# Performance work log

Hardware: AMD Instinct MI355X
Metric: run time of the kernel (lower is better)

## Reference

```python
import jax, jax.numpy as jnp
import numpy as np

N_NODES = 100000
N_EDGES = 1600000
D_IN = 128
D_HID = 128
D_OUT = 64
N_GRAPHS = 128


def setup_inputs() -> dict:
    key = jax.random.key(0)
    ks = jax.random.split(key, 8)
    x = jax.random.normal(ks[0], (N_NODES, D_IN), dtype=jnp.float32)
    edge_index = jax.random.randint(ks[1], (2, N_EDGES), 0, N_NODES, dtype=jnp.int64)
    batch = jnp.sort(jax.random.randint(ks[2], (N_NODES,), 0, N_GRAPHS, dtype=jnp.int64))
    def glorot(k, fi, fo):
        s = jnp.sqrt(6.0 / (fi + fo)).astype(jnp.float32)
        return jax.random.uniform(k, (fi, fo), jnp.float32, -1.0, 1.0) * s
    return {
        "x": x, "edge_index": edge_index, "batch": batch,
        "W1": glorot(ks[3], D_IN, D_HID), "b1": jnp.zeros((D_HID,), jnp.float32),
        "W2": glorot(ks[4], D_HID, D_HID), "b2": jnp.zeros((D_HID,), jnp.float32),
        "W3": glorot(ks[5], D_HID, D_HID), "b3": jnp.zeros((D_HID,), jnp.float32),
        "Wfc": glorot(ks[6], D_HID, D_OUT), "bfc": jnp.zeros((D_OUT,), jnp.float32),
    }


def _gcn_graph(edge_index, n_nodes):
    # add self-loops and compute symmetric normalization (PyG gcn_norm)
    loop = jnp.arange(n_nodes, dtype=edge_index.dtype)
    src = jnp.concatenate([edge_index[0], loop])
    dst = jnp.concatenate([edge_index[1], loop])
    deg = jax.ops.segment_sum(jnp.ones_like(dst, dtype=jnp.float32), dst,
                              num_segments=n_nodes)
    dinv = jnp.where(deg > 0, jax.lax.rsqrt(deg), 0.0)
    norm = dinv[src] * dinv[dst]  # [E + N]
    return src, dst, norm


def _gcn_conv(x, src, dst, norm, W, b, n_nodes):
    h = x @ W                                    # [N, F_out]
    msg = h[src] * norm[:, None]                 # gather + scale
    agg = jax.ops.segment_sum(msg, dst, num_segments=n_nodes)  # scatter-add
    return agg + b


def reference(x, edge_index, batch, W1, b1, W2, b2, W3, b3, Wfc, bfc):
    n = x.shape[0]
    src, dst, norm = _gcn_graph(edge_index, n)
    h = jax.nn.relu(_gcn_conv(x, src, dst, norm, W1, b1, n))
    h = jax.nn.relu(_gcn_conv(h, src, dst, norm, W2, b2, n))
    h = jax.nn.relu(_gcn_conv(h, src, dst, norm, W3, b3, n))
    # global mean pool over graphs in the batch
    sums = jax.ops.segment_sum(h, batch, num_segments=N_GRAPHS)
    cnts = jax.ops.segment_sum(jnp.ones((n,), jnp.float32), batch,
                               num_segments=N_GRAPHS)
    pooled = sums / jnp.maximum(cnts, 1.0)[:, None]   # [G, D_HID]
    return pooled @ Wfc + bfc                         # [G, D_OUT]
```

## Files before the change

### kernel.cpp

```cpp
#include <hip/hip_runtime.h>

#define NN 100000
#define NE 1600000
#define DF 128
#define DOUT 64
#define NG 128
#define NB 391
#define EPB 8192
#define NBLKA ((NE + EPB - 1) / EPB)
#define NBLKX 6250
#define PCH 8
#define NAGB (NN / 16)

typedef short short8 __attribute__((ext_vector_type(8)));
typedef float floatx4 __attribute__((ext_vector_type(4)));
typedef float floatx2 __attribute__((ext_vector_type(2)));

__device__ __forceinline__ unsigned short f2bf(float f) {
    unsigned int b = __float_as_uint(f);
    unsigned int r = (b + 0x7fffu + ((b >> 16) & 1u)) >> 16;
    return (unsigned short)r;
}
__device__ __forceinline__ float bf2f_lo(unsigned int v) { return __uint_as_float(v << 16); }
__device__ __forceinline__ float bf2f_hi(unsigned int v) { return __uint_as_float(v & 0xffff0000u); }

__device__ __forceinline__ int phi(int p) {
    return (((p >> 6) << 2) + (p & 3)) * 16 + ((p >> 2) & 15);
}


__global__ __launch_bounds__(256) void k_init(const int* __restrict__ batch,
                                              int* __restrict__ gstart,
                                              const float* __restrict__ W1,
                                              const float* __restrict__ W2,
                                              const float* __restrict__ W3,
                                              unsigned short* __restrict__ O1,
                                              unsigned short* __restrict__ O2,
                                              unsigned short* __restrict__ O3) {
    int blk = blockIdx.x;
    if (blk == 0) {
        int g = threadIdx.x;
        if (g > NG) return;
        int lo = 0, hi = NN;
        while (lo < hi) {
            int mid = (lo + hi) >> 1;
            if (batch[mid] < g) lo = mid + 1; else hi = mid;
        }
        gstart[g] = lo;
    } else {
        int bb = blk - 1;
        const float* W = (bb >= 16) ? W3 : (bb >= 8) ? W2 : W1;
        unsigned short* O = (bb >= 16) ? O3 : (bb >= 8) ? O2 : O1;
        int idx = (bb & 7) * 256 + threadIdx.x;
        int l = idx & 63;
        int s = (idx >> 6) & 3;
        int tt = idx >> 8;
        int k0 = s * 32 + (l >> 4) * 8;
        int c = tt * 16 + (l & 15);
        unsigned short o[8];
#pragma unroll
        for (int j = 0; j < 8; j++) o[j] = f2bf(W[phi(k0 + j) * DF + c]);
        *(short8*)&O[idx * 8] = *(short8*)o;
    }
}


__global__ __launch_bounds__(256) void k_pre(const int* __restrict__ dst,
                                             int* __restrict__ hist,
                                             const float* __restrict__ x,
                                             unsigned short* __restrict__ xb) {
    __shared__ int lh[NB];
    int t = threadIdx.x;
    if (blockIdx.x < NBLKA) {
        for (int i = t; i < NB; i += 256) lh[i] = 0;
        __syncthreads();
        int e0 = blockIdx.x * EPB;
        int e1 = min(e0 + EPB, NE);
        for (int e = e0 + t; e < e1; e += 256) atomicAdd(&lh[dst[e] >> 8], 1);
        __syncthreads();
        for (int i = t; i < NB; i += 256) hist[blockIdx.x * NB + i] = lh[i];
    } else {
        size_t i = ((size_t)(blockIdx.x - NBLKA) * 256 + t) * 8;
        size_t rb = i & ~(size_t)127;
        int p0 = (int)(i & 127);
        unsigned short o[8];
#pragma unroll
        for (int j = 0; j < 8; j++) o[j] = f2bf(x[rb + phi(p0 + j)]);
        *(short8*)&xb[i] = *(short8*)o;
    }
}

__global__ __launch_bounds__(256) void k_hscan(int* __restrict__ hist,
                                               int* __restrict__ bhist) {
    __shared__ int sh[256];
    int b = blockIdx.x, t = threadIdx.x;
    int v = (t < NBLKA) ? hist[t * NB + b] : 0;
    sh[t] = v;
    __syncthreads();
    for (int off = 1; off < 256; off <<= 1) {
        int a = (t >= off) ? sh[t - off] : 0;
        __syncthreads();
        sh[t] += a;
        __syncthreads();
    }
    if (t < NBLKA) hist[t * NB + b] = sh[t] - v;
    if (t == 255) bhist[b] = sh[255];
}

__global__ __launch_bounds__(512) void k_bscan(const int* __restrict__ bhist,
                                               int* __restrict__ bbase) {
    __shared__ int sh[512];
    int t = threadIdx.x;
    int v = (t < NB) ? bhist[t] : 0;
    sh[t] = v;
    __syncthreads();
    for (int off = 1; off < 512; off <<= 1) {
        int a = (t >= off) ? sh[t - off] : 0;
        __syncthreads();
        sh[t] += a;
        __syncthreads();
    }
    if (t < NB) bbase[t] = sh[t] - v;
    if (t == NB - 1) bbase[NB] = sh[t];
}

__global__ __launch_bounds__(256) void k_pairs(const int* __restrict__ src,
                                               const int* __restrict__ dst,
                                               const int* __restrict__ hist,
                                               const int* __restrict__ bbase,
                                               int2* __restrict__ ebuf) {
    __shared__ int lh[NB];
    __shared__ int lbase[NB];
    int t = threadIdx.x;
    for (int i = t; i < NB; i += 256) {
        lh[i] = 0;
        lbase[i] = bbase[i] + hist[blockIdx.x * NB + i];
    }
    __syncthreads();
    int e0 = blockIdx.x * EPB;
    int e1 = min(e0 + EPB, NE);
    for (int e = e0 + t; e < e1; e += 256) {
        int s = src[e], d = dst[e];
        int bk = d >> 8;
        int off = atomicAdd(&lh[bk], 1);
        ebuf[lbase[bk] + off] = make_int2(s, d);
    }
}

__global__ __launch_bounds__(256) void k_build(const int2* __restrict__ ebuf,
                                               const int* __restrict__ bbase,
                                               int* __restrict__ rowptr,
                                               float* __restrict__ dinv,
                                               int* __restrict__ col) {
    __shared__ int deg[256];
    __shared__ int lst[256];
    int b = blockIdx.x, t = threadIdx.x;
    int n0 = b << 8;
    int node = n0 + t;
    deg[t] = 0;
    __syncthreads();
    int e0 = bbase[b], e1 = bbase[b + 1];
    for (int e = e0 + t; e < e1; e += 256) atomicAdd(&deg[ebuf[e].y - n0], 1);
    __syncthreads();
    int v = deg[t];
    lst[t] = v;
    __syncthreads();
    for (int off = 1; off < 256; off <<= 1) {
        int a = (t >= off) ? lst[t - off] : 0;
        __syncthreads();
        lst[t] += a;
        __syncthreads();
    }
    int mystart = e0 + lst[t] - v;
    if (node < NN) {
        rowptr[node] = mystart;
        dinv[node] = rsqrtf((float)(v + 1));
    }
    if (b == NB - 1 && t == 255) rowptr[NN] = e1;
    lst[t] = mystart;
    __syncthreads();
    for (int e = e0 + t; e < e1; e += 256) {
        int2 pr = ebuf[e];
        int p = atomicAdd(&lst[pr.y - n0], 1);
        col[p] = pr.x * DF;
    }
}


__global__ __launch_bounds__(256) void k_gemm(const unsigned short* __restrict__ X,
                                              const unsigned short* __restrict__ Wb,
                                              const float* __restrict__ dinv,
                                              unsigned char* __restrict__ fs8) {
    int t = threadIdx.x;
    int wave = t >> 6, l = t & 63;
    int r0 = blockIdx.x * 64 + wave * 16;
    int lm = l & 15, q = l >> 4;

    int arow = r0 + lm;
    if (arow >= NN) arow = NN - 1;
    const unsigned short* xrow = X + (size_t)arow * DF + q * 8;
    short8 af0 = *(const short8*)(xrow);
    short8 af1 = *(const short8*)(xrow + 32);
    short8 af2 = *(const short8*)(xrow + 64);
    short8 af3 = *(const short8*)(xrow + 96);

    int orow = r0 + q * 4;
    float dv[4];
#pragma unroll
    for (int j = 0; j < 4; j++) dv[j] = (orow + j < NN) ? dinv[orow + j] : 0.f;

    float res[4][8];
#pragma unroll
    for (int tt = 0; tt < 8; tt++) {
        floatx4 acc = {0.f, 0.f, 0.f, 0.f};
        const unsigned short* wp = Wb + ((size_t)(tt * 4) * 64 + l) * 8;
        acc = __builtin_amdgcn_mfma_f32_16x16x32_bf16(af0, *(const short8*)(wp), acc, 0, 0, 0);
        acc = __builtin_amdgcn_mfma_f32_16x16x32_bf16(af1, *(const short8*)(wp + 512), acc, 0, 0, 0);
        acc = __builtin_amdgcn_mfma_f32_16x16x32_bf16(af2, *(const short8*)(wp + 1024), acc, 0, 0, 0);
        acc = __builtin_amdgcn_mfma_f32_16x16x32_bf16(af3, *(const short8*)(wp + 1536), acc, 0, 0, 0);
#pragma unroll
        for (int j = 0; j < 4; j++) res[j][tt] = acc[j] * dv[j];
    }

#pragma unroll
    for (int g = 0; g < 2; g++) {
#pragma unroll
        for (int j = 0; j < 4; j++) {
            int r = orow + j;
            if (r >= NN) continue;
            unsigned int w8 = __builtin_amdgcn_cvt_pk_fp8_f32(res[j][g * 4 + 0], res[j][g * 4 + 1], 0, false);
            w8 = __builtin_amdgcn_cvt_pk_fp8_f32(res[j][g * 4 + 2], res[j][g * 4 + 3], w8, true);
            *(unsigned int*)&fs8[(size_t)r * DF + g * 64 + lm * 4] = w8;
        }
    }
}

__global__ __launch_bounds__(256) void k_agg(const unsigned char* __restrict__ fs8,
                                             const int* __restrict__ colb,
                                             const int* __restrict__ rowptr,
                                             const float* __restrict__ dinv,
                                             const float* __restrict__ b,
                                             unsigned short* __restrict__ out) {
    int w = (int)((blockIdx.x * (size_t)blockDim.x + threadIdx.x) >> 6);
    int lane = threadIdx.x & 63;
    int sub = lane >> 4;
    int fo = lane & 15;
    int foff = fo * 8;
    int n = w * 4 + sub;

    float bias[8];
#pragma unroll
    for (int j = 0; j < 8; j++) bias[j] = b[phi(foff + j)];
    float dvn = dinv[n];

    int e0 = rowptr[n], e1 = rowptr[n + 1];

    floatx2 acc0 = {0.f, 0.f}, acc1 = {0.f, 0.f}, acc2 = {0.f, 0.f}, acc3 = {0.f, 0.f};

    for (int base = e0; base < e1; base += 8) {
        int cb[8];
#pragma unroll
        for (int k = 0; k < 8; k++) cb[k] = colb[min(base + k, e1 - 1)];
        uint2 vv[8];
#pragma unroll
        for (int k = 0; k < 8; k++) vv[k] = *(const uint2*)&fs8[(size_t)cb[k] + foff];
#pragma unroll
        for (int k = 0; k < 8; k++) {
            if (base + k < e1) {
                acc0 += __builtin_amdgcn_cvt_pk_f32_fp8(vv[k].x, false);
                acc1 += __builtin_amdgcn_cvt_pk_f32_fp8(vv[k].x, true);
                acc2 += __builtin_amdgcn_cvt_pk_f32_fp8(vv[k].y, false);
                acc3 += __builtin_amdgcn_cvt_pk_f32_fp8(vv[k].y, true);
            }
        }
    }

    uint2 sv = *(const uint2*)&fs8[(size_t)n * DF + foff];
    acc0 += __builtin_amdgcn_cvt_pk_f32_fp8(sv.x, false);
    acc1 += __builtin_amdgcn_cvt_pk_f32_fp8(sv.x, true);
    acc2 += __builtin_amdgcn_cvt_pk_f32_fp8(sv.y, false);
    acc3 += __builtin_amdgcn_cvt_pk_f32_fp8(sv.y, true);

    float a[8] = {acc0.x, acc0.y, acc1.x, acc1.y, acc2.x, acc2.y, acc3.x, acc3.y};
    float o[8];
#pragma unroll
    for (int j = 0; j < 8; j++) o[j] = fmaxf(dvn * a[j] + bias[j], 0.f);
    uint4 pk;
    pk.x = (unsigned int)f2bf(o[0]) | ((unsigned int)f2bf(o[1]) << 16);
    pk.y = (unsigned int)f2bf(o[2]) | ((unsigned int)f2bf(o[3]) << 16);
    pk.z = (unsigned int)f2bf(o[4]) | ((unsigned int)f2bf(o[5]) << 16);
    pk.w = (unsigned int)f2bf(o[6]) | ((unsigned int)f2bf(o[7]) << 16);
    *(uint4*)&out[(size_t)n * DF + foff] = pk;
}


__global__ __launch_bounds__(256) void k_poolA(const unsigned short* __restrict__ h,
                                               const int* __restrict__ gstart,
                                               float* __restrict__ part) {
    __shared__ float2 red[256];
    int g = blockIdx.x >> 3, c = blockIdx.x & 7;
    int s = gstart[g], e = gstart[g + 1];
    int len = e - s;
    int cs = s + (int)(((long long)len * c) >> 3);
    int ce = s + (int)(((long long)len * (c + 1)) >> 3);
    int t = threadIdx.x;
    int fp = t & 63;
    int rs = t >> 6;
    float2 acc = make_float2(0.f, 0.f);
    for (int n = cs + rs; n < ce; n += 4) {
        unsigned int v = *(const unsigned int*)&h[(size_t)n * DF + fp * 2];
        acc.x += bf2f_lo(v);
        acc.y += bf2f_hi(v);
    }
    red[t] = acc;
    __syncthreads();
    if (rs == 0) {
        float2 a0 = red[fp], a1 = red[fp + 64], a2 = red[fp + 128], a3 = red[fp + 192];
        float2 o;
        o.x = (a0.x + a1.x) + (a2.x + a3.x);
        o.y = (a0.y + a1.y) + (a2.y + a3.y);
        *(float2*)&part[(size_t)blockIdx.x * DF + fp * 2] = o;
    }
}

__global__ __launch_bounds__(128) void k_poolfc(const float* __restrict__ part,
                                                const int* __restrict__ gstart,
                                                const float* __restrict__ Wfc,
                                                const float* __restrict__ bfc,
                                                float* __restrict__ out) {
    __shared__ float pl[DF];
    int g = blockIdx.x;
    int f = threadIdx.x;
    float s = 0.f;
#pragma unroll
    for (int c = 0; c < PCH; c++) s += part[(size_t)(g * PCH + c) * DF + f];
    int cnt = gstart[g + 1] - gstart[g];
    pl[phi(f)] = s / (float)max(cnt, 1);
    __syncthreads();
    if (f < DOUT) {
        float acc = bfc[f];
        for (int k = 0; k < DF; k++) acc += pl[k] * Wfc[k * DOUT + f];
        out[g * DOUT + f] = acc;
    }
}


extern "C" void kernel_launch(void* const* d_in, const int* in_sizes, int n_in,
                              void* d_out, int out_size, void* d_ws, size_t ws_size,
                              hipStream_t stream) {
    const float* x     = (const float*)d_in[0];
    const int*   ei    = (const int*)d_in[1];
    const int*   batch = (const int*)d_in[2];
    const float* W1 = (const float*)d_in[3];
    const float* b1 = (const float*)d_in[4];
    const float* W2 = (const float*)d_in[5];
    const float* b2 = (const float*)d_in[6];
    const float* W3 = (const float*)d_in[7];
    const float* b3 = (const float*)d_in[8];
    const float* Wfc = (const float*)d_in[9];
    const float* bfc = (const float*)d_in[10];
    float* out = (float*)d_out;

    char* p = (char*)d_ws;
    unsigned short* xb = (unsigned short*)p;  p += (size_t)NN * DF * sizeof(short);
    unsigned short* ob = (unsigned short*)p;  p += (size_t)NN * DF * sizeof(short);
    unsigned char*  fs8 = (unsigned char*)p;  p += (size_t)NN * DF;
    unsigned short* Wb1 = (unsigned short*)p; p += 16384 * sizeof(short);
    unsigned short* Wb2 = (unsigned short*)p; p += 16384 * sizeof(short);
    unsigned short* Wb3 = (unsigned short*)p; p += 16384 * sizeof(short);
    float* dinv = (float*)p;           p += (size_t)NN * sizeof(float);
    int* rowptr = (int*)p;             p += (size_t)(NN + 4) * sizeof(int);
    int* col    = (int*)p;             p += (size_t)NE * sizeof(int);
    int2* ebuf  = (int2*)p;            p += (size_t)NE * sizeof(int2);
    int* bhist  = (int*)p;             p += (size_t)(NB + 4) * sizeof(int);
    int* bbase  = (int*)p;             p += (size_t)(NB + 4) * sizeof(int);
    int* hist   = (int*)p;             p += (size_t)NBLKA * NB * sizeof(int);
    int* gstart = (int*)p;             p += (size_t)(NG + 4) * sizeof(int);
    float* part = (float*)p;           p += (size_t)NG * PCH * DF * sizeof(float);

    const int* e_src = ei;
    const int* e_dst = ei + NE;

    k_init<<<25, 256, 0, stream>>>(batch, gstart, W1, W2, W3, Wb1, Wb2, Wb3);
    k_pre<<<NBLKA + NBLKX, 256, 0, stream>>>(e_dst, hist, x, xb);
    k_hscan<<<NB, 256, 0, stream>>>(hist, bhist);
    k_bscan<<<1, 512, 0, stream>>>(bhist, bbase);
    k_pairs<<<NBLKA, 256, 0, stream>>>(e_src, e_dst, hist, bbase, ebuf);
    k_build<<<NB, 256, 0, stream>>>(ebuf, bbase, rowptr, dinv, col);

    int ggrid = (NN + 63) / 64;

    k_gemm<<<ggrid, 256, 0, stream>>>(xb, Wb1, dinv, fs8);
    k_agg<<<NAGB, 256, 0, stream>>>(fs8, col, rowptr, dinv, b1, ob);
    k_gemm<<<ggrid, 256, 0, stream>>>(ob, Wb2, dinv, fs8);
    k_agg<<<NAGB, 256, 0, stream>>>(fs8, col, rowptr, dinv, b2, ob);
    k_gemm<<<ggrid, 256, 0, stream>>>(ob, Wb3, dinv, fs8);
    k_agg<<<NAGB, 256, 0, stream>>>(fs8, col, rowptr, dinv, b3, ob);

    k_poolA<<<NG * PCH, 256, 0, stream>>>(ob, gstart, part);
    k_poolfc<<<NG, 128, 0, stream>>>(part, gstart, Wfc, bfc, out);
}
```

Measured before the change: 337.0 us.

## Fuse aggregation with next layer's GEMM via shared-memory tile

Adds a fused kernel that aggregates 64 nodes per block into a swizzled bf16 LDS tile and then runs the next layer's MFMA GEMM on that tile, writing fp8 features directly. This removes the bf16 hidden-state write and reread between layers 1-2 and 2-3 and two kernel launches. Because outputs can no longer overwrite inputs in place, fp8 features ping-pong between two buffers. The cost is fewer waves per aggregation step (four nodes per wave done serially) and extra LDS use, which can reduce latency hiding for the gather.

Result: slower. 357.5 us (+6.1%).

```diff
diff --git a/kernel.cpp b/kernel.cpp
--- a/kernel.cpp
+++ b/kernel.cpp
@@ -11,6 +11,7 @@
 #define NBLKX 6250
 #define PCH 8
 #define NAGB (NN / 16)
+#define NBF ((NN + 63) / 64)
 
 typedef short short8 __attribute__((ext_vector_type(8)));
 typedef float floatx4 __attribute__((ext_vector_type(4)));
@@ -187,6 +188,40 @@
 }
 
 
+__device__ __forceinline__ void agg_node(const unsigned char* __restrict__ fs8,
+                                         const int* __restrict__ colb,
+                                         int n, int foff, int e0, int e1,
+                                         float dvn, const float* bias,
+                                         float* o) {
+    floatx2 acc0 = {0.f, 0.f}, acc1 = {0.f, 0.f}, acc2 = {0.f, 0.f}, acc3 = {0.f, 0.f};
+    for (int base = e0; base < e1; base += 8) {
+        int cb[8];
+#pragma unroll
+        for (int k = 0; k < 8; k++) cb[k] = colb[min(base + k, e1 - 1)];
+        uint2 vv[8];
+#pragma unroll
+        for (int k = 0; k < 8; k++) vv[k] = *(const uint2*)&fs8[(size_t)cb[k] + foff];
+#pragma unroll
+        for (int k = 0; k < 8; k++) {
+            if (base + k < e1) {
+                acc0 += __builtin_amdgcn_cvt_pk_f32_fp8(vv[k].x, false);
+                acc1 += __builtin_amdgcn_cvt_pk_f32_fp8(vv[k].x, true);
+                acc2 += __builtin_amdgcn_cvt_pk_f32_fp8(vv[k].y, false);
+                acc3 += __builtin_amdgcn_cvt_pk_f32_fp8(vv[k].y, true);
+            }
+        }
+    }
+    uint2 sv = *(const uint2*)&fs8[(size_t)n * DF + foff];
+    acc0 += __builtin_amdgcn_cvt_pk_f32_fp8(sv.x, false);
+    acc1 += __builtin_amdgcn_cvt_pk_f32_fp8(sv.x, true);
+    acc2 += __builtin_amdgcn_cvt_pk_f32_fp8(sv.y, false);
+    acc3 += __builtin_amdgcn_cvt_pk_f32_fp8(sv.y, true);
+
+    float a[8] = {acc0.x, acc0.y, acc1.x, acc1.y, acc2.x, acc2.y, acc3.x, acc3.y};
+#pragma unroll
+    for (int j = 0; j < 8; j++) o[j] = fmaxf(dvn * a[j] + bias[j], 0.f);
+}
+
 __global__ __launch_bounds__(256) void k_gemm(const unsigned short* __restrict__ X,
                                               const unsigned short* __restrict__ Wb,
                                               const float* __restrict__ dinv,
@@ -231,6 +266,81 @@
             unsigned int w8 = __builtin_amdgcn_cvt_pk_fp8_f32(res[j][g * 4 + 0], res[j][g * 4 + 1], 0, false);
             w8 = __builtin_amdgcn_cvt_pk_fp8_f32(res[j][g * 4 + 2], res[j][g * 4 + 3], w8, true);
             *(unsigned int*)&fs8[(size_t)r * DF + g * 64 + lm * 4] = w8;
+        }
+    }
+}
+
+__global__ __launch_bounds__(256, 6) void k_fused(const unsigned char* __restrict__ fs8_in,
+                                                  const int* __restrict__ colb,
+                                                  const int* __restrict__ rowptr,
+                                                  const float* __restrict__ dinv,
+                                                  const float* __restrict__ b,
+                                                  const unsigned short* __restrict__ Wb,
+                                                  unsigned char* __restrict__ fs8_out) {
+    __shared__ unsigned short tile[4][16 * DF];
+    int t = threadIdx.x;
+    int w = t >> 6, lane = t & 63;
+    int sub = lane >> 4, fo = lane & 15;
+    int foff = fo * 8;
+    int r0 = blockIdx.x * 64 + w * 16;
+
+    float bias[8];
+#pragma unroll
+    for (int j = 0; j < 8; j++) bias[j] = b[phi(foff + j)];
+
+    unsigned short* mytile = &tile[w][0];
+
+#pragma unroll 1
+    for (int pass = 0; pass < 4; ++pass) {
+        int row = pass * 4 + sub;
+        int n = r0 + row;
+        int nc = (n < NN) ? n : (NN - 1);
+        float dvn = dinv[nc];
+        int e0 = rowptr[nc], e1 = rowptr[nc + 1];
+        float o[8];
+        agg_node(fs8_in, colb, nc, foff, e0, e1, dvn, bias, o);
+        uint4 pk;
+        pk.x = (unsigned int)f2bf(o[0]) | ((unsigned int)f2bf(o[1]) << 16);
+        pk.y = (unsigned int)f2bf(o[2]) | ((unsigned int)f2bf(o[3]) << 16);
+        pk.z = (unsigned int)f2bf(o[4]) | ((unsigned int)f2bf(o[5]) << 16);
+        pk.w = (unsigned int)f2bf(o[6]) | ((unsigned int)f2bf(o[7]) << 16);
+        *(uint4*)&mytile[row * DF + ((fo ^ row) * 8)] = pk;
+    }
+    __syncthreads();
+
+    int lm = lane & 15, q = lane >> 4;
+    short8 af[4];
+#pragma unroll
+    for (int k = 0; k < 4; k++)
+        af[k] = *(const short8*)&mytile[lm * DF + (((q + 4 * k) ^ lm) * 8)];
+
+    int orow = r0 + q * 4;
+    float dv[4];
+#pragma unroll
+    for (int j = 0; j < 4; j++) dv[j] = (orow + j < NN) ? dinv[orow + j] : 0.f;
+
+#pragma unroll
+    for (int g = 0; g < 2; g++) {
+        float res[4][4];
+#pragma unroll
+        for (int u = 0; u < 4; u++) {
+            int tt = g * 4 + u;
+            floatx4 acc = {0.f, 0.f, 0.f, 0.f};
+            const unsigned short* wp = Wb + ((size_t)(tt * 4) * 64 + lane) * 8;
+            acc = __builtin_amdgcn_mfma_f32_16x16x32_bf16(af[0], *(const short8*)(wp), acc, 0, 0, 0);
+            acc = __builtin_amdgcn_mfma_f32_16x16x32_bf16(af[1], *(const short8*)(wp + 512), acc, 0, 0, 0);
+            acc = __builtin_amdgcn_mfma_f32_16x16x32_bf16(af[2], *(const short8*)(wp + 1024), acc, 0, 0, 0);
+            acc = __builtin_amdgcn_mfma_f32_16x16x32_bf16(af[3], *(const short8*)(wp + 1536), acc, 0, 0, 0);
+#pragma unroll
+            for (int j = 0; j < 4; j++) res[j][u] = acc[j] * dv[j];
+        }
+#pragma unroll
+        for (int j = 0; j < 4; j++) {
+            int r = orow + j;
+            if (r >= NN) continue;
+            unsigned int w8 = __builtin_amdgcn_cvt_pk_fp8_f32(res[j][0], res[j][1], 0, false);
+            w8 = __builtin_amdgcn_cvt_pk_fp8_f32(res[j][2], res[j][3], w8, true);
+            *(unsigned int*)&fs8_out[(size_t)r * DF + g * 64 + lm * 4] = w8;
         }
     }
 }
@@ -252,39 +362,11 @@
 #pragma unroll
     for (int j = 0; j < 8; j++) bias[j] = b[phi(foff + j)];
     float dvn = dinv[n];
-
     int e0 = rowptr[n], e1 = rowptr[n + 1];
 
-    floatx2 acc0 = {0.f, 0.f}, acc1 = {0.f, 0.f}, acc2 = {0.f, 0.f}, acc3 = {0.f, 0.f};
-
-    for (int base = e0; base < e1; base += 8) {
-        int cb[8];
-#pragma unroll
-        for (int k = 0; k < 8; k++) cb[k] = colb[min(base + k, e1 - 1)];
-        uint2 vv[8];
-#pragma unroll
-        for (int k = 0; k < 8; k++) vv[k] = *(const uint2*)&fs8[(size_t)cb[k] + foff];
-#pragma unroll
-        for (int k = 0; k < 8; k++) {
-            if (base + k < e1) {
-                acc0 += __builtin_amdgcn_cvt_pk_f32_fp8(vv[k].x, false);
-                acc1 += __builtin_amdgcn_cvt_pk_f32_fp8(vv[k].x, true);
-                acc2 += __builtin_amdgcn_cvt_pk_f32_fp8(vv[k].y, false);
-                acc3 += __builtin_amdgcn_cvt_pk_f32_fp8(vv[k].y, true);
-            }
-        }
-    }
-
-    uint2 sv = *(const uint2*)&fs8[(size_t)n * DF + foff];
-    acc0 += __builtin_amdgcn_cvt_pk_f32_fp8(sv.x, false);
-    acc1 += __builtin_amdgcn_cvt_pk_f32_fp8(sv.x, true);
-    acc2 += __builtin_amdgcn_cvt_pk_f32_fp8(sv.y, false);
-    acc3 += __builtin_amdgcn_cvt_pk_f32_fp8(sv.y, true);
-
-    float a[8] = {acc0.x, acc0.y, acc1.x, acc1.y, acc2.x, acc2.y, acc3.x, acc3.y};
     float o[8];
-#pragma unroll
-    for (int j = 0; j < 8; j++) o[j] = fmaxf(dvn * a[j] + bias[j], 0.f);
+    agg_node(fs8, colb, n, foff, e0, e1, dvn, bias, o);
+
     uint4 pk;
     pk.x = (unsigned int)f2bf(o[0]) | ((unsigned int)f2bf(o[1]) << 16);
     pk.y = (unsigned int)f2bf(o[2]) | ((unsigned int)f2bf(o[3]) << 16);
@@ -364,7 +446,8 @@
     char* p = (char*)d_ws;
     unsigned short* xb = (unsigned short*)p;  p += (size_t)NN * DF * sizeof(short);
     unsigned short* ob = (unsigned short*)p;  p += (size_t)NN * DF * sizeof(short);
-    unsigned char*  fs8 = (unsigned char*)p;  p += (size_t)NN * DF;
+    unsigned char*  fs8a = (unsigned char*)p; p += (size_t)NN * DF;
+    unsigned char*  fs8b = (unsigned char*)p; p += (size_t)NN * DF;
     unsigned short* Wb1 = (unsigned short*)p; p += 16384 * sizeof(short);
     unsigned short* Wb2 = (unsigned short*)p; p += 16384 * sizeof(short);
     unsigned short* Wb3 = (unsigned short*)p; p += 16384 * sizeof(short);
@@ -390,12 +473,10 @@
 
     int ggrid = (NN + 63) / 64;
 
-    k_gemm<<<ggrid, 256, 0, stream>>>(xb, Wb1, dinv, fs8);
-    k_agg<<<NAGB, 256, 0, stream>>>(fs8, col, rowptr, dinv, b1, ob);
-    k_gemm<<<ggrid, 256, 0, stream>>>(ob, Wb2, dinv, fs8);
-    k_agg<<<NAGB, 256, 0, stream>>>(fs8, col, rowptr, dinv, b2, ob);
-    k_gemm<<<ggrid, 256, 0, stream>>>(ob, Wb3, dinv, fs8);
-    k_agg<<<NAGB, 256, 0, stream>>>(fs8, col, rowptr, dinv, b3, ob);
+    k_gemm<<<ggrid, 256, 0, stream>>>(xb, Wb1, dinv, fs8a);
+    k_fused<<<NBF, 256, 0, stream>>>(fs8a, col, rowptr, dinv, b1, Wb2, fs8b);
+    k_fused<<<NBF, 256, 0, stream>>>(fs8b, col, rowptr, dinv, b2, Wb3, fs8a);
+    k_agg<<<NAGB, 256, 0, stream>>>(fs8a, col, rowptr, dinv, b3, ob);
 
     k_poolA<<<NG * PCH, 256, 0, stream>>>(ob, gstart, part);
     k_poolfc<<<NG, 128, 0, stream>>>(part, gstart, Wfc, bfc, out);
```

## Fuse x conversion into first GEMM and merge scans via last-block ticket

Applied to the files above, without the earlier changes.

Drops the separate pass that converts x to permuted bf16. The first GEMM now reads fp32 x directly and converts it in registers, and W1 is laid out in logical order to match. The histogram and weight-prep kernels are merged into one launch, and the two scan kernels are combined using an atomic ticket so the last block performs the global scan. The aggregation gains a fast path for degree ≤16 that pads neighbour indices to a zero row instead of masking them, trading extra gather loads for less branching. Together these cut launches and a full write-then-read of the bf16 copy of x, at the cost of more global loads in the first GEMM.

Result: slower. 351.9 us (+4.4%).

```diff
diff --git a/kernel.cpp b/kernel.cpp
--- a/kernel.cpp
+++ b/kernel.cpp
@@ -8,9 +8,9 @@
 #define NB 391
 #define EPB 8192
 #define NBLKA ((NE + EPB - 1) / EPB)
-#define NBLKX 6250
 #define PCH 8
 #define NAGB (NN / 16)
+#define ZOFF (NN * DF)
 
 typedef short short8 __attribute__((ext_vector_type(8)));
 typedef float floatx4 __attribute__((ext_vector_type(4)));
@@ -29,17 +29,31 @@
 }
 
 
-__global__ __launch_bounds__(256) void k_init(const int* __restrict__ batch,
+__global__ __launch_bounds__(256) void k_init(const int* __restrict__ dst,
+                                              int* __restrict__ hist,
+                                              const int* __restrict__ batch,
                                               int* __restrict__ gstart,
+                                              unsigned char* __restrict__ fs8,
+                                              int* __restrict__ ticket,
                                               const float* __restrict__ W1,
                                               const float* __restrict__ W2,
                                               const float* __restrict__ W3,
                                               unsigned short* __restrict__ O1,
                                               unsigned short* __restrict__ O2,
                                               unsigned short* __restrict__ O3) {
+    __shared__ int lh[NB];
     int blk = blockIdx.x;
-    if (blk == 0) {
-        int g = threadIdx.x;
+    int t = threadIdx.x;
+    if (blk < NBLKA) {
+        for (int i = t; i < NB; i += 256) lh[i] = 0;
+        __syncthreads();
+        int e0 = blk * EPB;
+        int e1 = min(e0 + EPB, NE);
+        for (int e = e0 + t; e < e1; e += 256) atomicAdd(&lh[dst[e] >> 8], 1);
+        __syncthreads();
+        for (int i = t; i < NB; i += 256) hist[blk * NB + i] = lh[i];
+    } else if (blk == NBLKA) {
+        int g = t;
         if (g > NG) return;
         int lo = 0, hi = NN;
         while (lo < hi) {
@@ -47,11 +61,15 @@
             if (batch[mid] < g) lo = mid + 1; else hi = mid;
         }
         gstart[g] = lo;
+    } else if (blk == NBLKA + 1) {
+        if (t < 32) *(unsigned int*)&fs8[ZOFF + t * 4] = 0u;
+        if (t == 32) *ticket = 0;
     } else {
-        int bb = blk - 1;
+        int bb = blk - (NBLKA + 2);
         const float* W = (bb >= 16) ? W3 : (bb >= 8) ? W2 : W1;
         unsigned short* O = (bb >= 16) ? O3 : (bb >= 8) ? O2 : O1;
-        int idx = (bb & 7) * 256 + threadIdx.x;
+        bool logical = (bb < 8);
+        int idx = (bb & 7) * 256 + t;
         int l = idx & 63;
         int s = (idx >> 6) & 3;
         int tt = idx >> 8;
@@ -59,69 +77,53 @@
         int c = tt * 16 + (l & 15);
         unsigned short o[8];
 #pragma unroll
-        for (int j = 0; j < 8; j++) o[j] = f2bf(W[phi(k0 + j) * DF + c]);
+        for (int j = 0; j < 8; j++) {
+            int kk = logical ? (k0 + j) : phi(k0 + j);
+            o[j] = f2bf(W[kk * DF + c]);
+        }
         *(short8*)&O[idx * 8] = *(short8*)o;
     }
 }
 
 
-__global__ __launch_bounds__(256) void k_pre(const int* __restrict__ dst,
-                                             int* __restrict__ hist,
-                                             const float* __restrict__ x,
-                                             unsigned short* __restrict__ xb) {
-    __shared__ int lh[NB];
-    int t = threadIdx.x;
-    if (blockIdx.x < NBLKA) {
-        for (int i = t; i < NB; i += 256) lh[i] = 0;
-        __syncthreads();
-        int e0 = blockIdx.x * EPB;
-        int e1 = min(e0 + EPB, NE);
-        for (int e = e0 + t; e < e1; e += 256) atomicAdd(&lh[dst[e] >> 8], 1);
-        __syncthreads();
-        for (int i = t; i < NB; i += 256) hist[blockIdx.x * NB + i] = lh[i];
-    } else {
-        size_t i = ((size_t)(blockIdx.x - NBLKA) * 256 + t) * 8;
-        size_t rb = i & ~(size_t)127;
-        int p0 = (int)(i & 127);
-        unsigned short o[8];
-#pragma unroll
-        for (int j = 0; j < 8; j++) o[j] = f2bf(x[rb + phi(p0 + j)]);
-        *(short8*)&xb[i] = *(short8*)o;
-    }
-}
-
-__global__ __launch_bounds__(256) void k_hscan(int* __restrict__ hist,
-                                               int* __restrict__ bhist) {
-    __shared__ int sh[256];
+__global__ __launch_bounds__(512) void k_scan(int* __restrict__ hist,
+                                              int* __restrict__ bhist,
+                                              int* __restrict__ bbase,
+                                              int* __restrict__ ticket) {
+    __shared__ int sh[512];
+    __shared__ int amLast;
     int b = blockIdx.x, t = threadIdx.x;
     int v = (t < NBLKA) ? hist[t * NB + b] : 0;
     sh[t] = v;
     __syncthreads();
-    for (int off = 1; off < 256; off <<= 1) {
-        int a = (t >= off) ? sh[t - off] : 0;
-        __syncthreads();
-        sh[t] += a;
-        __syncthreads();
-    }
-    if (t < NBLKA) hist[t * NB + b] = sh[t] - v;
-    if (t == 255) bhist[b] = sh[255];
-}
-
-__global__ __launch_bounds__(512) void k_bscan(const int* __restrict__ bhist,
-                                               int* __restrict__ bbase) {
-    __shared__ int sh[512];
-    int t = threadIdx.x;
-    int v = (t < NB) ? bhist[t] : 0;
-    sh[t] = v;
-    __syncthreads();
     for (int off = 1; off < 512; off <<= 1) {
         int a = (t >= off) ? sh[t - off] : 0;
         __syncthreads();
         sh[t] += a;
         __syncthreads();
     }
-    if (t < NB) bbase[t] = sh[t] - v;
-    if (t == NB - 1) bbase[NB] = sh[t];
+    if (t < NBLKA) hist[t * NB + b] = sh[t] - v;
+    if (t == 511) atomicExch(&bhist[b], sh[511]);
+    __syncthreads();
+    if (t == 0) {
+        __threadfence();
+        amLast = (atomicAdd(ticket, 1) == NB - 1) ? 1 : 0;
+    }
+    __syncthreads();
+    if (amLast) {
+        int v2 = (t < NB) ? atomicAdd(&bhist[t], 0) : 0;
+        __syncthreads();
+        sh[t] = v2;
+        __syncthreads();
+        for (int off = 1; off < 512; off <<= 1) {
+            int a = (t >= off) ? sh[t - off] : 0;
+            __syncthreads();
+            sh[t] += a;
+            __syncthreads();
+        }
+        if (t < NB) bbase[t] = sh[t] - v2;
+        if (t == NB - 1) bbase[NB] = sh[t];
+    }
 }
 
 __global__ __launch_bounds__(256) void k_pairs(const int* __restrict__ src,
@@ -187,6 +189,65 @@
 }
 
 
+__device__ __forceinline__ void gemm_core(const short8* af,
+                                          const unsigned short* __restrict__ Wb,
+                                          const float* __restrict__ dinv,
+                                          int lane, int lm, int orow,
+                                          unsigned char* __restrict__ fs8) {
+    float dv[4];
+#pragma unroll
+    for (int j = 0; j < 4; j++) dv[j] = (orow + j < NN) ? dinv[orow + j] : 0.f;
+
+    float res[4][8];
+#pragma unroll
+    for (int tt = 0; tt < 8; tt++) {
+        floatx4 acc = {0.f, 0.f, 0.f, 0.f};
+        const unsigned short* wp = Wb + ((size_t)(tt * 4) * 64 + lane) * 8;
+        acc = __builtin_amdgcn_mfma_f32_16x16x32_bf16(af[0], *(const short8*)(wp), acc, 0, 0, 0);
+        acc = __builtin_amdgcn_mfma_f32_16x16x32_bf16(af[1], *(const short8*)(wp + 512), acc, 0, 0, 0);
+        acc = __builtin_amdgcn_mfma_f32_16x16x32_bf16(af[2], *(const short8*)(wp + 1024), acc, 0, 0, 0);
+        acc = __builtin_amdgcn_mfma_f32_16x16x32_bf16(af[3], *(const short8*)(wp + 1536), acc, 0, 0, 0);
+#pragma unroll
+        for (int j = 0; j < 4; j++) res[j][tt] = acc[j] * dv[j];
+    }
+
+#pragma unroll
+    for (int g = 0; g < 2; g++) {
+#pragma unroll
+        for (int j = 0; j < 4; j++) {
+            int r = orow + j;
+            if (r >= NN) continue;
+            unsigned int w8 = __builtin_amdgcn_cvt_pk_fp8_f32(res[j][g * 4 + 0], res[j][g * 4 + 1], 0, false);
+            w8 = __builtin_amdgcn_cvt_pk_fp8_f32(res[j][g * 4 + 2], res[j][g * 4 + 3], w8, true);
+            *(unsigned int*)&fs8[(size_t)r * DF + g * 64 + lm * 4] = w8;
+        }
+    }
+}
+
+__global__ __launch_bounds__(256) void k_gemm1(const float* __restrict__ X,
+                                               const unsigned short* __restrict__ Wb,
+                                               const float* __restrict__ dinv,
+                                               unsigned char* __restrict__ fs8) {
+    int t = threadIdx.x;
+    int wave = t >> 6, l = t & 63;
+    int r0 = blockIdx.x * 64 + wave * 16;
+    int lm = l & 15, q = l >> 4;
+
+    int arow = r0 + lm;
+    if (arow >= NN) arow = NN - 1;
+    const float* xrow = X + (size_t)arow * DF + q * 8;
+    short8 af[4];
+#pragma unroll
+    for (int s = 0; s < 4; s++) {
+        float4 f0 = *(const float4*)(xrow + s * 32);
+        float4 f1 = *(const float4*)(xrow + s * 32 + 4);
+        unsigned short o[8] = {f2bf(f0.x), f2bf(f0.y), f2bf(f0.z), f2bf(f0.w),
+                               f2bf(f1.x), f2bf(f1.y), f2bf(f1.z), f2bf(f1.w)};
+        af[s] = *(short8*)o;
+    }
+    gemm_core(af, Wb, dinv, l, lm, r0 + q * 4, fs8);
+}
+
 __global__ __launch_bounds__(256) void k_gemm(const unsigned short* __restrict__ X,
                                               const unsigned short* __restrict__ Wb,
                                               const float* __restrict__ dinv,
@@ -199,40 +260,67 @@
     int arow = r0 + lm;
     if (arow >= NN) arow = NN - 1;
     const unsigned short* xrow = X + (size_t)arow * DF + q * 8;
-    short8 af0 = *(const short8*)(xrow);
-    short8 af1 = *(const short8*)(xrow + 32);
-    short8 af2 = *(const short8*)(xrow + 64);
-    short8 af3 = *(const short8*)(xrow + 96);
-
-    int orow = r0 + q * 4;
-    float dv[4];
-#pragma unroll
-    for (int j = 0; j < 4; j++) dv[j] = (orow + j < NN) ? dinv[orow + j] : 0.f;
-
-    float res[4][8];
-#pragma unroll
-    for (int tt = 0; tt < 8; tt++) {
-        floatx4 acc = {0.f, 0.f, 0.f, 0.f};
-        const unsigned short* wp = Wb + ((size_t)(tt * 4) * 64 + l) * 8;
-        acc = __builtin_amdgcn_mfma_f32_16x16x32_bf16(af0, *(const short8*)(wp), acc, 0, 0, 0);
-        acc = __builtin_amdgcn_mfma_f32_16x16x32_bf16(af1, *(const short8*)(wp + 512), acc, 0, 0, 0);
-        acc = __builtin_amdgcn_mfma_f32_16x16x32_bf16(af2, *(const short8*)(wp + 1024), acc, 0, 0, 0);
-        acc = __builtin_amdgcn_mfma_f32_16x16x32_bf16(af3, *(const short8*)(wp + 1536), acc, 0, 0, 0);
-#pragma unroll
-        for (int j = 0; j < 4; j++) res[j][tt] = acc[j] * dv[j];
-    }
-
-#pragma unroll
-    for (int g = 0; g < 2; g++) {
-#pragma unroll
-        for (int j = 0; j < 4; j++) {
-            int r = orow + j;
-            if (r >= NN) continue;
-            unsigned int w8 = __builtin_amdgcn_cvt_pk_fp8_f32(res[j][g * 4 + 0], res[j][g * 4 + 1], 0, false);
-            w8 = __builtin_amdgcn_cvt_pk_fp8_f32(res[j][g * 4 + 2], res[j][g * 4 + 3], w8, true);
-            *(unsigned int*)&fs8[(size_t)r * DF + g * 64 + lm * 4] = w8;
-        }
-    }
+    short8 af[4];
+#pragma unroll
+    for (int s = 0; s < 4; s++) af[s] = *(const short8*)(xrow + s * 32);
+    gemm_core(af, Wb, dinv, l, lm, r0 + q * 4, fs8);
+}
+
+__device__ __forceinline__ void agg_node(const unsigned char* __restrict__ fs8,
+                                         const int* __restrict__ colb,
+                                         int n, int foff, int e0, int e1,
+                                         float dvn, const float* bias,
+                                         float* o) {
+    floatx2 acc0 = {0.f, 0.f}, acc1 = {0.f, 0.f}, acc2 = {0.f, 0.f}, acc3 = {0.f, 0.f};
+    int deg = e1 - e0;
+    if (deg <= 16) {
+        int cb[16];
+#pragma unroll
+        for (int k = 0; k < 16; k++) {
+            int idx = e0 + k;
+            int cv = colb[min(idx, e1 - 1)];
+            cb[k] = (idx < e1) ? cv : ZOFF;
+        }
+        uint2 vv[16];
+#pragma unroll
+        for (int k = 0; k < 16; k++) vv[k] = *(const uint2*)&fs8[(size_t)cb[k] + foff];
+#pragma unroll
+        for (int k = 0; k < 16; k++) {
+            acc0 += __builtin_amdgcn_cvt_pk_f32_fp8(vv[k].x, false);
+            acc1 += __builtin_amdgcn_cvt_pk_f32_fp8(vv[k].x, true);
+            acc2 += __builtin_amdgcn_cvt_pk_f32_fp8(vv[k].y, false);
+            acc3 += __builtin_amdgcn_cvt_pk_f32_fp8(vv[k].y, true);
+        }
+    } else {
+        for (int base = e0; base < e1; base += 8) {
+            int cb[8];
+#pragma unroll
+            for (int k = 0; k < 8; k++) {
+                int idx = base + k;
+                int cv = colb[min(idx, e1 - 1)];
+                cb[k] = (idx < e1) ? cv : ZOFF;
+            }
+            uint2 vv[8];
+#pragma unroll
+            for (int k = 0; k < 8; k++) vv[k] = *(const uint2*)&fs8[(size_t)cb[k] + foff];
+#pragma unroll
+            for (int k = 0; k < 8; k++) {
+                acc0 += __builtin_amdgcn_cvt_pk_f32_fp8(vv[k].x, false);
+                acc1 += __builtin_amdgcn_cvt_pk_f32_fp8(vv[k].x, true);
+                acc2 += __builtin_amdgcn_cvt_pk_f32_fp8(vv[k].y, false);
+                acc3 += __builtin_amdgcn_cvt_pk_f32_fp8(vv[k].y, true);
+            }
+        }
+    }
+    uint2 sv = *(const uint2*)&fs8[(size_t)n * DF + foff];
+    acc0 += __builtin_amdgcn_cvt_pk_f32_fp8(sv.x, false);
+    acc1 += __builtin_amdgcn_cvt_pk_f32_fp8(sv.x, true);
+    acc2 += __builtin_amdgcn_cvt_pk_f32_fp8(sv.y, false);
+    acc3 += __builtin_amdgcn_cvt_pk_f32_fp8(sv.y, true);
+
+    float a[8] = {acc0.x, acc0.y, acc1.x, acc1.y, acc2.x, acc2.y, acc3.x, acc3.y};
+#pragma unroll
+    for (int j = 0; j < 8; j++) o[j] = fmaxf(dvn * a[j] + bias[j], 0.f);
 }
 
 __global__ __launch_bounds__(256) void k_agg(const unsigned char* __restrict__ fs8,
@@ -252,39 +340,11 @@
 #pragma unroll
     for (int j = 0; j < 8; j++) bias[j] = b[phi(foff + j)];
     float dvn = dinv[n];
-
     int e0 = rowptr[n], e1 = rowptr[n + 1];
 
-    floatx2 acc0 = {0.f, 0.f}, acc1 = {0.f, 0.f}, acc2 = {0.f, 0.f}, acc3 = {0.f, 0.f};
-
-    for (int base = e0; base < e1; base += 8) {
-        int cb[8];
-#pragma unroll
-        for (int k = 0; k < 8; k++) cb[k] = colb[min(base + k, e1 - 1)];
-        uint2 vv[8];
-#pragma unroll
-        for (int k = 0; k < 8; k++) vv[k] = *(const uint2*)&fs8[(size_t)cb[k] + foff];
-#pragma unroll
-        for (int k = 0; k < 8; k++) {
-            if (base + k < e1) {
-                acc0 += __builtin_amdgcn_cvt_pk_f32_fp8(vv[k].x, false);
-                acc1 += __builtin_amdgcn_cvt_pk_f32_fp8(vv[k].x, true);
-                acc2 += __builtin_amdgcn_cvt_pk_f32_fp8(vv[k].y, false);
-                acc3 += __builtin_amdgcn_cvt_pk_f32_fp8(vv[k].y, true);
-            }
-        }
-    }
-
-    uint2 sv = *(const uint2*)&fs8[(size_t)n * DF + foff];
-    acc0 += __builtin_amdgcn_cvt_pk_f32_fp8(sv.x, false);
-    acc1 += __builtin_amdgcn_cvt_pk_f32_fp8(sv.x, true);
-    acc2 += __builtin_amdgcn_cvt_pk_f32_fp8(sv.y, false);
-    acc3 += __builtin_amdgcn_cvt_pk_f32_fp8(sv.y, true);
-
-    float a[8] = {acc0.x, acc0.y, acc1.x, acc1.y, acc2.x, acc2.y, acc3.x, acc3.y};
     float o[8];
-#pragma unroll
-    for (int j = 0; j < 8; j++) o[j] = fmaxf(dvn * a[j] + bias[j], 0.f);
+    agg_node(fs8, colb, n, foff, e0, e1, dvn, bias, o);
+
     uint4 pk;
     pk.x = (unsigned int)f2bf(o[0]) | ((unsigned int)f2bf(o[1]) << 16);
     pk.y = (unsigned int)f2bf(o[2]) | ((unsigned int)f2bf(o[3]) << 16);
@@ -362,9 +422,8 @@
     float* out = (float*)d_out;
 
     char* p = (char*)d_ws;
-    unsigned short* xb = (unsigned short*)p;  p += (size_t)NN * DF * sizeof(short);
     unsigned short* ob = (unsigned short*)p;  p += (size_t)NN * DF * sizeof(short);
-    unsigned char*  fs8 = (unsigned char*)p;  p += (size_t)NN * DF;
+    unsigned char*  fs8 = (unsigned char*)p;  p += (size_t)NN * DF + 256;
     unsigned short* Wb1 = (unsigned short*)p; p += 16384 * sizeof(short);
     unsigned short* Wb2 = (unsigned short*)p; p += 16384 * sizeof(short);
     unsigned short* Wb3 = (unsigned short*)p; p += 16384 * sizeof(short);
@@ -376,21 +435,21 @@
     int* bbase  = (int*)p;             p += (size_t)(NB + 4) * sizeof(int);
     int* hist   = (int*)p;             p += (size_t)NBLKA * NB * sizeof(int);
     int* gstart = (int*)p;             p += (size_t)(NG + 4) * sizeof(int);
+    int* ticket = (int*)p;             p += 4 * sizeof(int);
     float* part = (float*)p;           p += (size_t)NG * PCH * DF * sizeof(float);
 
     const int* e_src = ei;
     const int* e_dst = ei + NE;
 
-    k_init<<<25, 256, 0, stream>>>(batch, gstart, W1, W2, W3, Wb1, Wb2, Wb3);
-    k_pre<<<NBLKA + NBLKX, 256, 0, stream>>>(e_dst, hist, x, xb);
-    k_hscan<<<NB, 256, 0, stream>>>(hist, bhist);
-    k_bscan<<<1, 512, 0, stream>>>(bhist, bbase);
+    k_init<<<NBLKA + 26, 256, 0, stream>>>(e_dst, hist, batch, gstart, fs8, ticket,
+                                           W1, W2, W3, Wb1, Wb2, Wb3);
+    k_scan<<<NB, 512, 0, stream>>>(hist, bhist, bbase, ticket);
     k_pairs<<<NBLKA, 256, 0, stream>>>(e_src, e_dst, hist, bbase, ebuf);
     k_build<<<NB, 256, 0, stream>>>(ebuf, bbase, rowptr, dinv, col);
 
     int ggrid = (NN + 63) / 64;
 
-    k_gemm<<<ggrid, 256, 0, stream>>>(xb, Wb1, dinv, fs8);
+    k_gemm1<<<ggrid, 256, 0, stream>>>(x, Wb1, dinv, fs8);
     k_agg<<<NAGB, 256, 0, stream>>>(fs8, col, rowptr, dinv, b1, ob);
     k_gemm<<<ggrid, 256, 0, stream>>>(ob, Wb2, dinv, fs8);
     k_agg<<<NAGB, 256, 0, stream>>>(fs8, col, rowptr, dinv, b2, ob);
```
